# Kernel optimization log

Measured on AMD Instinct MI355X. Metric: run time of the kernel, lower is better.

## Reference

```python
import jax, jax.numpy as jnp
import numpy as np

LN2 = jnp.log(jnp.float32(2.0))
ALPHA = 0.5          # alpha_pool = [0.5]
A_BITS = 8           # activation bit width (BIT_TYPE_A)
W_BITS = 8           # weight bit width (BIT_TYPE_W)
EPS = 1e-8


def round_ln(x):
    # 'round' branch: floor(log2(x)) then pick nearer power of two
    y = jnp.floor(jnp.log(x) / LN2)
    up = (x - 2.0 ** y) > (2.0 ** (y + 1.0) - x)
    return y + up.astype(x.dtype)


def fq_act_asym(x, bits=A_BITS):
    # per-tensor asymmetric uniform fake-quant (QAct min-max observer)
    qmax = 2 ** bits - 1
    xmin = jnp.minimum(x.min(), 0.0)
    xmax = jnp.maximum(x.max(), 0.0)
    scale = jnp.maximum((xmax - xmin) / qmax, EPS)
    zp = jnp.round(-xmin / scale)
    q = jnp.clip(jnp.round(x / scale) + zp, 0, qmax)
    return (q - zp) * scale


def fq_act_sym(x, bits=A_BITS):
    # per-tensor symmetric fake-quant (qact1 with asymmetric=False)
    qmax = 2 ** (bits - 1) - 1
    scale = jnp.maximum(jnp.abs(x).max() / qmax, EPS)
    q = jnp.clip(jnp.round(x / scale), -qmax - 1, qmax)
    return q * scale


def fq_weight(w, bits=W_BITS):
    # per-output-channel symmetric weight fake-quant (QLinear)
    qmax = 2 ** (bits - 1) - 1
    scale = jnp.maximum(jnp.abs(w).max(axis=1, keepdims=True) / qmax, EPS)
    q = jnp.clip(jnp.round(w / scale), -qmax - 1, qmax)
    return q * scale


def setup_inputs() -> dict:
    key = jax.random.key(0)
    ks = jax.random.split(key, 5)
    B, N, C, H = 64, 197, 768, 3072
    x = jax.random.normal(ks[0], (B, N, C), dtype=jnp.float32)
    w1 = jax.random.normal(ks[1], (H, C), dtype=jnp.float32) * 0.02
    b1 = jax.random.normal(ks[2], (H,), dtype=jnp.float32) * 0.02
    w2 = jax.random.normal(ks[3], (C, H), dtype=jnp.float32) * 0.02
    b2 = jax.random.normal(ks[4], (C,), dtype=jnp.float32) * 0.02
    return {"x": x, "w1": w1, "b1": b1, "w2": w2, "b2": b2}


def reference(x, w1, b1, w2, b2):
    # ---- smoothquant power-of-two channel scale (fc1 input channels) ----
    global_max_x = jnp.abs(x).max(axis=(0, 1))      # [C]
    max_weight = jnp.abs(w1).max(axis=0)            # [C]
    cs = global_max_x ** ALPHA / max_weight ** (1.0 - ALPHA)
    cs = 2.0 ** round_ln(cs)                        # snap to power of two
    x_smoothed = x / cs[None, None, :]
    w1_smoothed = w1 * cs[None, :]
    # ---- qact0 -> fc1 (8-bit fake-quant GEMM) ----
    xq = fq_act_asym(x_smoothed)
    h = jnp.einsum('bnc,hc->bnh', xq, fq_weight(w1_smoothed)) + b1
    # ---- act (exact GELU, nn.GELU default) -> qact1 (symmetric) ----
    h = jax.nn.gelu(h, approximate=False)
    hq = fq_act_sym(h)
    # ---- fc2 -> qact2 ----
    out = jnp.einsum('bnh,ch->bnc', hq, fq_weight(w2)) + b2
    out = fq_act_asym(out)
    return out
```

## Files before the change

kernel.cpp:

```cpp
#include <hip/hip_runtime.h>
#include <cstdint>
#include <cstddef>

typedef int v4i __attribute__((ext_vector_type(4)));

#define DI static __device__ __forceinline__

DI unsigned fmap(float f){ unsigned b=__float_as_uint(f); return (b&0x80000000u)? ~b : (b|0x80000000u); }
DI float funmap(unsigned u){ return (u&0x80000000u)? __uint_as_float(u&0x7fffffffu) : __uint_as_float(~u); }
DI float gelu_f(float x){ return 0.5f*x*(1.0f+erff(x*0.70710678118654752440f)); }

constexpr int Mtok = 12608;
constexpr int Cdim = 768;
constexpr int Hdim = 3072;
constexpr int MP   = 12672;

__global__ void k_init(unsigned* scal, unsigned* xminU, unsigned* xmaxU, unsigned* wmaxU){
    int t = blockIdx.x*256 + threadIdx.x;
    if (t < Cdim){
        xminU[t] = fmap(__builtin_inff());
        xmaxU[t] = fmap(-__builtin_inff());
        wmaxU[t] = fmap(0.0f);
    }
    if (t == 0){
        scal[0] = fmap(0.0f);
        scal[1] = fmap(__builtin_inff());
        scal[2] = fmap(-__builtin_inff());
    }
}

__global__ void k_colstats_x(const float* __restrict__ x, unsigned* xminU, unsigned* xmaxU){
    int t = threadIdx.x;
    float mn0= __builtin_inff(), mn1= __builtin_inff(), mn2= __builtin_inff();
    float mx0=-__builtin_inff(), mx1=-__builtin_inff(), mx2=-__builtin_inff();
    for (int r = blockIdx.x; r < Mtok; r += gridDim.x){
        const float* row = x + (size_t)r*Cdim;
        float v0=row[t], v1=row[t+256], v2=row[t+512];
        mn0=fminf(mn0,v0); mx0=fmaxf(mx0,v0);
        mn1=fminf(mn1,v1); mx1=fmaxf(mx1,v1);
        mn2=fminf(mn2,v2); mx2=fmaxf(mx2,v2);
    }
    atomicMin(&xminU[t      ], fmap(mn0)); atomicMax(&xmaxU[t      ], fmap(mx0));
    atomicMin(&xminU[t+256  ], fmap(mn1)); atomicMax(&xmaxU[t+256  ], fmap(mx1));
    atomicMin(&xminU[t+512  ], fmap(mn2)); atomicMax(&xmaxU[t+512  ], fmap(mx2));
}

__global__ void k_colmax_w1(const float* __restrict__ w1, unsigned* wmaxU){
    int t = threadIdx.x;
    float m0=0.f, m1=0.f, m2=0.f;
    for (int r = blockIdx.x; r < Hdim; r += gridDim.x){
        const float* row = w1 + (size_t)r*Cdim;
        m0=fmaxf(m0,fabsf(row[t]));
        m1=fmaxf(m1,fabsf(row[t+256]));
        m2=fmaxf(m2,fabsf(row[t+512]));
    }
    atomicMax(&wmaxU[t      ], fmap(m0));
    atomicMax(&wmaxU[t+256  ], fmap(m1));
    atomicMax(&wmaxU[t+512  ], fmap(m2));
}

__global__ void k_scale0(const unsigned* xminU, const unsigned* xmaxU, const unsigned* wmaxU,
                         float* cs, unsigned* scal){
    __shared__ float smn[256], smx[256];
    int t = threadIdx.x;
    float lmn =  __builtin_inff(), lmx = -__builtin_inff();
    #pragma unroll
    for (int j = 0; j < 3; ++j){
        int c = t + j*256;
        float xn = funmap(xminU[c]), xm = funmap(xmaxU[c]), wm = funmap(wmaxU[c]);
        float g  = fmaxf(fabsf(xn), fabsf(xm));
        float csr = powf(g, 0.5f) / powf(wm, 0.5f);
        float y = floorf(logf(csr) / 0.6931471805599453f);
        float p = exp2f(y);
        float c2 = exp2f(y + (((csr - p) > (2.0f*p - csr)) ? 1.0f : 0.0f));
        cs[c] = c2;
        lmn = fminf(lmn, xn / c2);
        lmx = fmaxf(lmx, xm / c2);
    }
    smn[t]=lmn; smx[t]=lmx; __syncthreads();
    for (int s=128; s; s>>=1){
        if (t < s){ smn[t]=fminf(smn[t],smn[t+s]); smx[t]=fmaxf(smx[t],smx[t+s]); }
        __syncthreads();
    }
    if (t == 0){
        float xmin_t = fminf(smn[0], 0.0f);
        float xmax_t = fmaxf(smx[0], 0.0f);
        float sc = fmaxf((xmax_t - xmin_t)/255.0f, 1e-8f);
        float zp = rintf(-xmin_t/sc);
        float* fs = (float*)scal;
        fs[8] = sc; fs[9] = zp;
    }
}

__global__ void k_quant_w1(const float* __restrict__ w1, const float* __restrict__ cs,
                           const unsigned* scal, int8_t* __restrict__ qw1,
                           float* sa1, int* icorr1){
    __shared__ float sm[256];
    __shared__ int   si[256];
    int h = blockIdx.x, t = threadIdx.x;
    const float* wr = w1 + (size_t)h*Cdim;
    float v0 = wr[t]*cs[t], v1 = wr[t+256]*cs[t+256], v2 = wr[t+512]*cs[t+512];
    float am = fmaxf(fabsf(v0), fmaxf(fabsf(v1), fabsf(v2)));
    sm[t]=am; __syncthreads();
    for (int s=128; s; s>>=1){ if (t<s) sm[t]=fmaxf(sm[t],sm[t+s]); __syncthreads(); }
    float scale = fmaxf(sm[0]/127.0f, 1e-8f);
    float q0 = fminf(fmaxf(rintf(v0/scale), -128.0f), 127.0f);
    float q1 = fminf(fmaxf(rintf(v1/scale), -128.0f), 127.0f);
    float q2 = fminf(fmaxf(rintf(v2/scale), -128.0f), 127.0f);
    qw1[(size_t)h*Cdim + t      ] = (int8_t)q0;
    qw1[(size_t)h*Cdim + t + 256] = (int8_t)q1;
    qw1[(size_t)h*Cdim + t + 512] = (int8_t)q2;
    si[t] = (int)q0 + (int)q1 + (int)q2; __syncthreads();
    for (int s=128; s; s>>=1){ if (t<s) si[t]+=si[t+s]; __syncthreads(); }
    if (t == 0){
        const float* fs = (const float*)scal;
        sa1[h]    = fs[8]*scale;
        icorr1[h] = (128 - (int)fs[9]) * si[0];
    }
}

__global__ void k_quant_w2(const float* __restrict__ w2, int8_t* __restrict__ qw2, float* sa2){
    __shared__ float sm[256];
    int c = blockIdx.x, t = threadIdx.x;
    const float* wr = w2 + (size_t)c*Hdim;
    float v[12]; float am = 0.f;
    #pragma unroll
    for (int j=0;j<12;++j){ v[j]=wr[t + j*256]; am=fmaxf(am,fabsf(v[j])); }
    sm[t]=am; __syncthreads();
    for (int s=128; s; s>>=1){ if (t<s) sm[t]=fmaxf(sm[t],sm[t+s]); __syncthreads(); }
    float scale = fmaxf(sm[0]/127.0f, 1e-8f);
    #pragma unroll
    for (int j=0;j<12;++j){
        float q = fminf(fmaxf(rintf(v[j]/scale), -128.0f), 127.0f);
        qw2[(size_t)c*Hdim + t + j*256] = (int8_t)q;
    }
    if (t == 0) sa2[c] = scale;
}

__global__ void k_quant_x(const float* __restrict__ x, const float* __restrict__ cs,
                          const unsigned* scal, int8_t* __restrict__ qxs){
    int idx = blockIdx.x*256 + threadIdx.x;
    const int total = Mtok*(Cdim/4);
    if (idx >= total) return;
    const float* fs = (const float*)scal;
    float sc = fs[8], zp = fs[9];
    float4 v = ((const float4*)x)[idx];
    int cb = (idx % (Cdim/4))*4;
    float q0 = fminf(fmaxf(rintf((v.x/cs[cb+0])/sc)+zp, 0.f), 255.f);
    float q1 = fminf(fmaxf(rintf((v.y/cs[cb+1])/sc)+zp, 0.f), 255.f);
    float q2 = fminf(fmaxf(rintf((v.z/cs[cb+2])/sc)+zp, 0.f), 255.f);
    float q3 = fminf(fmaxf(rintf((v.w/cs[cb+3])/sc)+zp, 0.f), 255.f);
    uint32_t pack =  (uint32_t)(uint8_t)((int)q0-128)
                  | ((uint32_t)(uint8_t)((int)q1-128) << 8)
                  | ((uint32_t)(uint8_t)((int)q2-128) << 16)
                  | ((uint32_t)(uint8_t)((int)q3-128) << 24);
    ((uint32_t*)qxs)[idx] = pack;
}

#define GLL(src,dst) __builtin_amdgcn_global_load_lds( \
    (const __attribute__((address_space(1))) unsigned*)(src), \
    (__attribute__((address_space(3))) unsigned*)(dst), 16, 0, 0)

template<int KSTEPS, int MODE, int NY>
__global__ __launch_bounds__(256)
void k_gemm(const int8_t* __restrict__ A, const int8_t* __restrict__ Bw, int N,
            const float* __restrict__ sa, const int* __restrict__ icorr,
            const float* __restrict__ bias, const unsigned* __restrict__ scal,
            int8_t* __restrict__ qout, float* __restrict__ fout, _Float16* __restrict__ hout,
            unsigned* __restrict__ r0, unsigned* __restrict__ r1)
{
    constexpr int K = KSTEPS*64;
    __shared__ __align__(16) int8_t LDSB[24576];
    __shared__ float sred[8];
    int t = threadIdx.x, lane = t & 63, wid = t >> 6;
    int wr = wid >> 1, wc = wid & 1;

    int nwg = gridDim.x;
    int q8 = nwg >> 3, r8 = nwg & 7;
    int xcd = blockIdx.x & 7, li = blockIdx.x >> 3;
    int swz = (xcd < r8 ? xcd*(q8+1) : r8*(q8+1) + (xcd - r8)*q8) + li;
    int bx = swz / NY, by = swz % NY;
    size_t brow = (size_t)bx * 128;
    int bcol = by * 128;

    int srow = t >> 2;
    int schunk = (t & 3) ^ ((srow >> 1) & 3);
    const int8_t* ga0 = A  + (brow + srow)*(size_t)K + schunk*16;

    const int8_t* gB = Bw + (size_t)(bcol + wc*64 + (lane & 15))*K + ((lane >> 4) << 4);

    int rsw  = ((lane >> 4) ^ ((lane >> 1) & 3)) << 4;
    int aoff = ((wr*64 + (lane & 15)) << 6) + rsw;

    float sav[4], bbv[4]; int icv[4]; float sh = 0.f;
    #pragma unroll
    for (int n=0;n<4;++n){
        int col = bcol + wc*64 + n*16 + (lane & 15);
        sav[n] = sa[col];
        bbv[n] = bias[col];
        icv[n] = (MODE == 2) ? 0 : icorr[col];
    }
    if (MODE == 1 || MODE == 2) sh = fmaxf(funmap(*scal)/127.0f, 1e-8f);
    asm volatile("" ::: "memory");

#define STAGE(sb, ks) do{ \
    const int8_t* pa_ = ga0 + (ks)*64; \
    int8_t* ld_ = LDSB + (sb)*8192 + t*16; \
    GLL(pa_,                ld_); \
    GLL(pa_ + (size_t)64*K, ld_ + 4096); \
}while(0)

    v4i acc[4][4] = {};
    v4i bcur[4];

    STAGE(0,0);
    __builtin_amdgcn_sched_barrier(0);
    #pragma unroll
    for (int n=0;n<4;++n) bcur[n] = *(const v4i*)(gB + (size_t)n*(16*K));
    __builtin_amdgcn_sched_barrier(0);
    STAGE(1,1);

#define ITER(cur, ks, WAITN, HASB, HASSTAGE) do{ \
    asm volatile("s_waitcnt vmcnt(" #WAITN ")" ::: "memory"); \
    __builtin_amdgcn_s_barrier(); \
    v4i bn_[4]; \
    if (HASB){ \
        _Pragma("unroll") \
        for (int n_=0;n_<4;++n_) bn_[n_] = *(const v4i*)(gB + (size_t)n_*(16*K) + ((ks)+1)*64); \
    } \
    __builtin_amdgcn_sched_barrier(0); \
    if (HASSTAGE) STAGE(((cur)+2)%3, (ks)+2); \
    const int8_t* bp_ = LDSB + (cur)*8192; \
    v4i a_[4]; \
    _Pragma("unroll") \
    for (int m_=0;m_<4;++m_) a_[m_] = *(const v4i*)(bp_ + aoff + (m_<<10)); \
    asm volatile("s_waitcnt lgkmcnt(0)" ::: "memory"); \
    __builtin_amdgcn_sched_barrier(0); \
    __builtin_amdgcn_s_setprio(1); \
    _Pragma("unroll") \
    for (int m_=0;m_<4;++m_) \
        _Pragma("unroll") \
        for (int n_=0;n_<4;++n_) \
            acc[m_][n_] = __builtin_amdgcn_mfma_i32_16x16x64_i8(a_[m_], bcur[n_], acc[m_][n_], 0, 0, 0); \
    __builtin_amdgcn_s_setprio(0); \
    if (HASB){ \
        _Pragma("unroll") \
        for (int n_=0;n_<4;++n_) bcur[n_] = bn_[n_]; \
    } \
}while(0)

    constexpr int MAING = KSTEPS/3 - 1;
    for (int kg = 0; kg < MAING; ++kg){
        int ks = kg*3;
        ITER(0, ks,   2, true, true);
        ITER(1, ks+1, 2, true, true);
        ITER(2, ks+2, 2, true, true);
    }
    ITER(0, KSTEPS-3, 2, true,  true);
    ITER(1, KSTEPS-2, 2, true,  false);
    ITER(2, KSTEPS-1, 0, false, false);
#undef ITER
#undef STAGE

    int rl = (lane >> 4) * 4;
    if (MODE == 0){
        float amax = 0.f;
        #pragma unroll
        for (int n=0;n<4;++n){
            #pragma unroll
            for (int m=0;m<4;++m){
                size_t row = brow + wr*64 + m*16 + rl;
                #pragma unroll
                for (int r=0;r<4;++r){
                    if (row + r < (size_t)Mtok){
                        float g = gelu_f(sav[n]*(float)(acc[m][n][r] + icv[n]) + bbv[n]);
                        amax = fmaxf(amax, fabsf(g));
                    }
                }
            }
        }
        #pragma unroll
        for (int off=32; off; off>>=1) amax = fmaxf(amax, __shfl_down(amax, off));
        if (lane == 0) sred[wid] = amax;
        __syncthreads();
        if (t == 0) atomicMax(r0, fmap(fmaxf(fmaxf(sred[0],sred[1]), fmaxf(sred[2],sred[3]))));
    } else if (MODE == 1){
        #pragma unroll
        for (int n=0;n<4;++n){
            int col = bcol + wc*64 + n*16 + (lane & 15);
            #pragma unroll
            for (int m=0;m<4;++m){
                size_t row = brow + wr*64 + m*16 + rl;
                #pragma unroll
                for (int r=0;r<4;++r){
                    if (row + r < (size_t)Mtok){
                        float g = gelu_f(sav[n]*(float)(acc[m][n][r] + icv[n]) + bbv[n]);
                        float qv = fminf(fmaxf(rintf(g/sh), -128.0f), 127.0f);
                        qout[(row + r)*(size_t)N + col] = (int8_t)qv;
                    }
                }
            }
        }
    } else if (MODE == 3){
        float amax = 0.f;
        _Float16* hb = hout + ((size_t)(bx*NY + by))*16384 + wid*4096 + lane*4;
        #pragma unroll
        for (int n=0;n<4;++n){
            #pragma unroll
            for (int m=0;m<4;++m){
                size_t row = brow + wr*64 + m*16 + rl;
                union { _Float16 h4[4]; uint2 u2; } pk;
                #pragma unroll
                for (int r=0;r<4;++r){
                    float g = gelu_f(sav[n]*(float)(acc[m][n][r] + icv[n]) + bbv[n]);
                    if (row + r < (size_t)Mtok) amax = fmaxf(amax, fabsf(g));
                    pk.h4[r] = (_Float16)g;
                }
                *(uint2*)(hb + (n*4+m)*256) = pk.u2;
            }
        }
        #pragma unroll
        for (int off=32; off; off>>=1) amax = fmaxf(amax, __shfl_down(amax, off));
        if (lane == 0) sred[wid] = amax;
        __syncthreads();
        if (t == 0) atomicMax(r0, fmap(fmaxf(fmaxf(sred[0],sred[1]), fmaxf(sred[2],sred[3]))));
    } else {
        float lmin =  __builtin_inff(), lmax = -__builtin_inff();
        float* ob = fout + ((size_t)(bx*NY + by))*16384 + wid*4096 + lane*4;
        #pragma unroll
        for (int n=0;n<4;++n){
            float s = sh * sav[n];
            #pragma unroll
            for (int m=0;m<4;++m){
                size_t row = brow + wr*64 + m*16 + rl;
                float4 o4;
                #pragma unroll
                for (int r=0;r<4;++r){
                    float o = s*(float)acc[m][n][r] + bbv[n];
                    if (row + r < (size_t)Mtok){ lmin = fminf(lmin, o); lmax = fmaxf(lmax, o); }
                    ((float*)&o4)[r] = o;
                }
                *(float4*)(ob + (n*4+m)*256) = o4;
            }
        }
        #pragma unroll
        for (int off=32; off; off>>=1){
            lmin = fminf(lmin, __shfl_down(lmin, off));
            lmax = fmaxf(lmax, __shfl_down(lmax, off));
        }
        if (lane == 0){ sred[wid] = lmin; sred[4+wid] = lmax; }
        __syncthreads();
        if (t == 0){
            atomicMin(r0, fmap(fminf(fminf(sred[0],sred[1]), fminf(sred[2],sred[3]))));
            atomicMax(r1, fmap(fmaxf(fmaxf(sred[4],sred[5]), fmaxf(sred[6],sred[7]))));
        }
    }
}

__global__ void k_requant(const _Float16* __restrict__ h, const unsigned* __restrict__ scal,
                          int8_t* __restrict__ qh){
    int idx = blockIdx.x*256 + threadIdx.x;
    const int total = Mtok*(Hdim/8);
    if (idx >= total) return;
    float sh = fmaxf(funmap(scal[0])/127.0f, 1e-8f);
    int R  = idx / 384;
    int cb = (idx - R*384) * 8;
    int bx = R >> 7, r0 = R & 127;
    int by = cb >> 7, c0 = cb & 127;
    int wid2 = (r0 >> 6)*2 + (c0 >> 6);
    int m = (r0 >> 4) & 3, n = (c0 >> 4) & 3;
    int lane2 = ((r0 >> 2) & 3)*16 + (c0 & 15);
    int r = r0 & 3;
    const _Float16* p = h + ((size_t)(bx*24 + by))*16384 + wid2*4096 + (n*4+m)*256 + lane2*4 + r;
    uint32_t lo = 0, hi = 0;
    #pragma unroll
    for (int j=0;j<4;++j){
        float q = fminf(fmaxf(rintf((float)p[4*j]/sh), -128.0f), 127.0f);
        lo |= ((uint32_t)(uint8_t)(int)q) << (8*j);
    }
    #pragma unroll
    for (int j=0;j<4;++j){
        float q = fminf(fmaxf(rintf((float)p[4*(4+j)]/sh), -128.0f), 127.0f);
        hi |= ((uint32_t)(uint8_t)(int)q) << (8*j);
    }
    uint2 pk; pk.x = lo; pk.y = hi;
    ((uint2*)qh)[idx] = pk;
}

__global__ void k_final(const float* __restrict__ outpre, const unsigned* __restrict__ scal,
                        float* __restrict__ out){
    int idx = blockIdx.x*256 + threadIdx.x;
    const int total = Mtok*(Cdim/4);
    if (idx >= total) return;
    float omin = fminf(funmap(scal[1]), 0.0f);
    float omax = fmaxf(funmap(scal[2]), 0.0f);
    float sc = fmaxf((omax - omin)/255.0f, 1e-8f);
    float zp = rintf(-omin/sc);
    int R  = idx / 192;
    int cb = (idx - R*192) * 4;
    int bx = R >> 7, r0 = R & 127;
    int by = cb >> 7, c0 = cb & 127;
    int wid2 = (r0 >> 6)*2 + (c0 >> 6);
    int m = (r0 >> 4) & 3, n = (c0 >> 4) & 3;
    int lane2 = ((r0 >> 2) & 3)*16 + (c0 & 15);
    int r = r0 & 3;
    const float* p = outpre + ((size_t)(bx*6 + by))*16384 + wid2*4096 + (n*4+m)*256 + lane2*4 + r;
    float4 v;
    v.x = p[0]; v.y = p[4]; v.z = p[8]; v.w = p[12];
    v.x = (fminf(fmaxf(rintf(v.x/sc)+zp, 0.f), 255.f) - zp)*sc;
    v.y = (fminf(fmaxf(rintf(v.y/sc)+zp, 0.f), 255.f) - zp)*sc;
    v.z = (fminf(fmaxf(rintf(v.z/sc)+zp, 0.f), 255.f) - zp)*sc;
    v.w = (fminf(fmaxf(rintf(v.w/sc)+zp, 0.f), 255.f) - zp)*sc;
    ((float4*)out)[idx] = v;
}

extern "C" void kernel_launch(void* const* d_in, const int* in_sizes, int n_in,
                              void* d_out, int out_size, void* d_ws, size_t ws_size,
                              hipStream_t stream)
{
    if (n_in < 5) return;
    const float* x  = (const float*)d_in[0];
    const float* w1 = (const float*)d_in[1];
    const float* b1 = (const float*)d_in[2];
    const float* w2 = (const float*)d_in[3];
    const float* b2 = (const float*)d_in[4];
    float* out = (float*)d_out;

    uint8_t* w = (uint8_t*)d_ws;
    size_t off = 0;
    unsigned* scal  = (unsigned*)(w + off); off += 256;
    unsigned* xminU = (unsigned*)(w + off); off += 3072;
    unsigned* xmaxU = (unsigned*)(w + off); off += 3072;
    unsigned* wmaxU = (unsigned*)(w + off); off += 3072;
    float*    cs    = (float*)   (w + off); off += 3072;
    float*    sa1   = (float*)   (w + off); off += 12288;
    int*      icorr1= (int*)     (w + off); off += 12288;
    float*    sa2   = (float*)   (w + off); off += 3072;
    off = (off + 255) & ~(size_t)255;
    int8_t*   qw1   = (int8_t*)  (w + off); off += (size_t)Hdim*Cdim;
    int8_t*   qw2   = (int8_t*)  (w + off); off += (size_t)Cdim*Hdim;
    int8_t*   qxs   = (int8_t*)  (w + off); off += (size_t)MP*Cdim;
    int8_t*   qh    = (int8_t*)  (w + off); off += (size_t)MP*Hdim;
    size_t off_big = off;
    float*    outpre= (float*)   (w + off_big);
    _Float16* hbuf  = (_Float16*)(w + off_big);
    size_t need_3g  = off_big + (size_t)99*6*16384*4;
    size_t need_h16 = off_big + (size_t)99*24*16384*2;
    if (ws_size < need_3g) return;
    bool use_h16 = (ws_size >= need_h16);

    k_init<<<3, 256, 0, stream>>>(scal, xminU, xmaxU, wmaxU);
    k_colstats_x<<<512, 256, 0, stream>>>(x, xminU, xmaxU);
    k_colmax_w1<<<512, 256, 0, stream>>>(w1, wmaxU);
    k_scale0<<<1, 256, 0, stream>>>(xminU, xmaxU, wmaxU, cs, scal);
    k_quant_w1<<<Hdim, 256, 0, stream>>>(w1, cs, scal, qw1, sa1, icorr1);
    k_quant_w2<<<Cdim, 256, 0, stream>>>(w2, qw2, sa2);
    k_quant_x<<<(Mtok*(Cdim/4) + 255)/256, 256, 0, stream>>>(x, cs, scal, qxs);

    if (use_h16){
        k_gemm<12,3,24><<<2376, 256, 0, stream>>>(qxs, qw1, Hdim, sa1, icorr1, b1, scal,
                                                  nullptr, nullptr, hbuf, &scal[0], nullptr);
        k_requant<<<(Mtok*(Hdim/8) + 255)/256, 256, 0, stream>>>(hbuf, scal, qh);
    } else {
        k_gemm<12,0,24><<<2376, 256, 0, stream>>>(qxs, qw1, Hdim, sa1, icorr1, b1, scal,
                                                  nullptr, nullptr, nullptr, &scal[0], nullptr);
        k_gemm<12,1,24><<<2376, 256, 0, stream>>>(qxs, qw1, Hdim, sa1, icorr1, b1, scal,
                                                  qh, nullptr, nullptr, nullptr, nullptr);
    }
    k_gemm<48,2,6><<<594, 256, 0, stream>>>(qh, qw2, Cdim, sa2, nullptr, b2, scal,
                                            nullptr, outpre, nullptr, &scal[1], &scal[2]);

    k_final<<<(Mtok*(Cdim/4) + 255)/256, 256, 0, stream>>>(outpre, scal, out);
}
```

Measured before the change: 442.5 us.

## Replace triple-buffered GEMM pipeline with double-buffered 128-K stages and fast erf

Replaces the hand-scheduled three-stage LDS pipeline (64-wide K steps, explicit vmcnt waits, register-prefetched B) with a simpler double-buffered loop over 128-wide K stages, using an XOR swizzle across 8 chunks and __syncthreads between stages. It also adds a launch-bounds occupancy hint of 3 blocks per CU and swaps erff for an Abramowitz-Stegun polynomial erf in GELU. The aim is fewer barriers per K and cheaper epilogue math. The cost is less fine-grained overlap, with B loads no longer prefetched a step ahead, and an erf approximation with about 1e-7 error that could flip rounding on a few quantized values.

```diff
diff --git a/kernel.cpp b/kernel.cpp
--- a/kernel.cpp
+++ b/kernel.cpp
@@ -8,7 +8,15 @@
 
 DI unsigned fmap(float f){ unsigned b=__float_as_uint(f); return (b&0x80000000u)? ~b : (b|0x80000000u); }
 DI float funmap(unsigned u){ return (u&0x80000000u)? __uint_as_float(u&0x7fffffffu) : __uint_as_float(~u); }
-DI float gelu_f(float x){ return 0.5f*x*(1.0f+erff(x*0.70710678118654752440f)); }
+
+DI float erf_fast(float x){
+    float ax = fabsf(x);
+    float t  = __builtin_amdgcn_rcpf(1.0f + 0.3275911f*ax);
+    float p  = t*(0.254829592f + t*(-0.284496736f + t*(1.421413741f + t*(-1.453152027f + t*1.061405429f))));
+    float r  = 1.0f - p*__expf(-ax*ax);
+    return copysignf(r, x);
+}
+DI float gelu_f(float x){ return 0.5f*x*(1.0f + erf_fast(x*0.70710678118654752440f)); }
 
 constexpr int Mtok = 12608;
 constexpr int Cdim = 768;
@@ -161,19 +169,20 @@
     (const __attribute__((address_space(1))) unsigned*)(src), \
     (__attribute__((address_space(3))) unsigned*)(dst), 16, 0, 0)
 
-template<int KSTEPS, int MODE, int NY>
-__global__ __launch_bounds__(256)
+template<int KDIM, int MODE, int NY>
+__global__ __launch_bounds__(256, 3)
 void k_gemm(const int8_t* __restrict__ A, const int8_t* __restrict__ Bw, int N,
             const float* __restrict__ sa, const int* __restrict__ icorr,
             const float* __restrict__ bias, const unsigned* __restrict__ scal,
             int8_t* __restrict__ qout, float* __restrict__ fout, _Float16* __restrict__ hout,
             unsigned* __restrict__ r0, unsigned* __restrict__ r1)
 {
-    constexpr int K = KSTEPS*64;
-    __shared__ __align__(16) int8_t LDSB[24576];
+    constexpr int NST = KDIM/128;
+    __shared__ __align__(16) int8_t LDSB[2][16384];
     __shared__ float sred[8];
     int t = threadIdx.x, lane = t & 63, wid = t >> 6;
     int wr = wid >> 1, wc = wid & 1;
+    int l15 = lane & 15, lhi = lane >> 4, l7 = lane & 7;
 
     int nwg = gridDim.x;
     int q8 = nwg >> 3, r8 = nwg & 7;
@@ -183,86 +192,66 @@
     size_t brow = (size_t)bx * 128;
     int bcol = by * 128;
 
-    int srow = t >> 2;
-    int schunk = (t & 3) ^ ((srow >> 1) & 3);
-    const int8_t* ga0 = A  + (brow + srow)*(size_t)K + schunk*16;
-
-    const int8_t* gB = Bw + (size_t)(bcol + wc*64 + (lane & 15))*K + ((lane >> 4) << 4);
-
-    int rsw  = ((lane >> 4) ^ ((lane >> 1) & 3)) << 4;
-    int aoff = ((wr*64 + (lane & 15)) << 6) + rsw;
+    int srow   = t >> 3;
+    int schunk = (t & 7) ^ (srow & 7);
+    const int8_t* ga0 = A + (size_t)(brow + srow)*KDIM + schunk*16;
+
+    const int8_t* gB = Bw + (size_t)(bcol + wc*64 + l15)*KDIM + (lhi << 4);
+
+    int arow = (wr*64 + l15) * 128;
 
     float sav[4], bbv[4]; int icv[4]; float sh = 0.f;
     #pragma unroll
     for (int n=0;n<4;++n){
-        int col = bcol + wc*64 + n*16 + (lane & 15);
+        int col = bcol + wc*64 + n*16 + l15;
         sav[n] = sa[col];
         bbv[n] = bias[col];
         icv[n] = (MODE == 2) ? 0 : icorr[col];
     }
     if (MODE == 1 || MODE == 2) sh = fmaxf(funmap(*scal)/127.0f, 1e-8f);
-    asm volatile("" ::: "memory");
-
-#define STAGE(sb, ks) do{ \
-    const int8_t* pa_ = ga0 + (ks)*64; \
-    int8_t* ld_ = LDSB + (sb)*8192 + t*16; \
-    GLL(pa_,                ld_); \
-    GLL(pa_ + (size_t)64*K, ld_ + 4096); \
+
+#define STAGE(buf, s) do{ \
+    const int8_t* p_ = ga0 + (size_t)(s)*128; \
+    int8_t* l_ = LDSB[buf] + t*16; \
+    GLL(p_,                   l_); \
+    GLL(p_ + (size_t)32*KDIM, l_ + 4096); \
+    GLL(p_ + (size_t)64*KDIM, l_ + 8192); \
+    GLL(p_ + (size_t)96*KDIM, l_ + 12288); \
 }while(0)
 
     v4i acc[4][4] = {};
-    v4i bcur[4];
-
-    STAGE(0,0);
-    __builtin_amdgcn_sched_barrier(0);
-    #pragma unroll
-    for (int n=0;n<4;++n) bcur[n] = *(const v4i*)(gB + (size_t)n*(16*K));
-    __builtin_amdgcn_sched_barrier(0);
-    STAGE(1,1);
-
-#define ITER(cur, ks, WAITN, HASB, HASSTAGE) do{ \
-    asm volatile("s_waitcnt vmcnt(" #WAITN ")" ::: "memory"); \
-    __builtin_amdgcn_s_barrier(); \
-    v4i bn_[4]; \
-    if (HASB){ \
-        _Pragma("unroll") \
-        for (int n_=0;n_<4;++n_) bn_[n_] = *(const v4i*)(gB + (size_t)n_*(16*K) + ((ks)+1)*64); \
-    } \
-    __builtin_amdgcn_sched_barrier(0); \
-    if (HASSTAGE) STAGE(((cur)+2)%3, (ks)+2); \
-    const int8_t* bp_ = LDSB + (cur)*8192; \
-    v4i a_[4]; \
-    _Pragma("unroll") \
-    for (int m_=0;m_<4;++m_) a_[m_] = *(const v4i*)(bp_ + aoff + (m_<<10)); \
-    asm volatile("s_waitcnt lgkmcnt(0)" ::: "memory"); \
-    __builtin_amdgcn_sched_barrier(0); \
-    __builtin_amdgcn_s_setprio(1); \
-    _Pragma("unroll") \
-    for (int m_=0;m_<4;++m_) \
-        _Pragma("unroll") \
-        for (int n_=0;n_<4;++n_) \
-            acc[m_][n_] = __builtin_amdgcn_mfma_i32_16x16x64_i8(a_[m_], bcur[n_], acc[m_][n_], 0, 0, 0); \
-    __builtin_amdgcn_s_setprio(0); \
-    if (HASB){ \
-        _Pragma("unroll") \
-        for (int n_=0;n_<4;++n_) bcur[n_] = bn_[n_]; \
-    } \
-}while(0)
-
-    constexpr int MAING = KSTEPS/3 - 1;
-    for (int kg = 0; kg < MAING; ++kg){
-        int ks = kg*3;
-        ITER(0, ks,   2, true, true);
-        ITER(1, ks+1, 2, true, true);
-        ITER(2, ks+2, 2, true, true);
-    }
-    ITER(0, KSTEPS-3, 2, true,  true);
-    ITER(1, KSTEPS-2, 2, true,  false);
-    ITER(2, KSTEPS-1, 0, false, false);
-#undef ITER
+    STAGE(0, 0);
+    __syncthreads();
+
+    for (int s = 0; s < NST; ++s){
+        int cur = s & 1;
+        v4i bb[4][2];
+        #pragma unroll
+        for (int n=0;n<4;++n)
+            #pragma unroll
+            for (int kc=0;kc<2;++kc)
+                bb[n][kc] = *(const v4i*)(gB + (size_t)n*(16*KDIM) + s*128 + kc*64);
+        if (s + 1 < NST) STAGE(cur^1, s+1);
+        v4i aa[4][2];
+        #pragma unroll
+        for (int m=0;m<4;++m)
+            #pragma unroll
+            for (int kc=0;kc<2;++kc)
+                aa[m][kc] = *(const v4i*)(LDSB[cur] + arow + (m<<11) + (((kc*4 + lhi) ^ l7) << 4));
+        __builtin_amdgcn_s_setprio(1);
+        #pragma unroll
+        for (int kc=0;kc<2;++kc)
+            #pragma unroll
+            for (int m=0;m<4;++m)
+                #pragma unroll
+                for (int n=0;n<4;++n)
+                    acc[m][n] = __builtin_amdgcn_mfma_i32_16x16x64_i8(aa[m][kc], bb[n][kc], acc[m][n], 0, 0, 0);
+        __builtin_amdgcn_s_setprio(0);
+        __syncthreads();
+    }
 #undef STAGE
 
-    int rl = (lane >> 4) * 4;
+    int rl = lhi * 4;
     if (MODE == 0){
         float amax = 0.f;
         #pragma unroll
@@ -287,7 +276,7 @@
     } else if (MODE == 1){
         #pragma unroll
         for (int n=0;n<4;++n){
-            int col = bcol + wc*64 + n*16 + (lane & 15);
+            int col = bcol + wc*64 + n*16 + l15;
             #pragma unroll
             for (int m=0;m<4;++m){
                 size_t row = brow + wr*64 + m*16 + rl;
@@ -458,17 +447,17 @@
     k_quant_x<<<(Mtok*(Cdim/4) + 255)/256, 256, 0, stream>>>(x, cs, scal, qxs);
 
     if (use_h16){
-        k_gemm<12,3,24><<<2376, 256, 0, stream>>>(qxs, qw1, Hdim, sa1, icorr1, b1, scal,
-                                                  nullptr, nullptr, hbuf, &scal[0], nullptr);
+        k_gemm<768,3,24><<<2376, 256, 0, stream>>>(qxs, qw1, Hdim, sa1, icorr1, b1, scal,
+                                                   nullptr, nullptr, hbuf, &scal[0], nullptr);
         k_requant<<<(Mtok*(Hdim/8) + 255)/256, 256, 0, stream>>>(hbuf, scal, qh);
     } else {
-        k_gemm<12,0,24><<<2376, 256, 0, stream>>>(qxs, qw1, Hdim, sa1, icorr1, b1, scal,
-                                                  nullptr, nullptr, nullptr, &scal[0], nullptr);
-        k_gemm<12,1,24><<<2376, 256, 0, stream>>>(qxs, qw1, Hdim, sa1, icorr1, b1, scal,
-                                                  qh, nullptr, nullptr, nullptr, nullptr);
-    }
-    k_gemm<48,2,6><<<594, 256, 0, stream>>>(qh, qw2, Cdim, sa2, nullptr, b2, scal,
-                                            nullptr, outpre, nullptr, &scal[1], &scal[2]);
+        k_gemm<768,0,24><<<2376, 256, 0, stream>>>(qxs, qw1, Hdim, sa1, icorr1, b1, scal,
+                                                   nullptr, nullptr, nullptr, &scal[0], nullptr);
+        k_gemm<768,1,24><<<2376, 256, 0, stream>>>(qxs, qw1, Hdim, sa1, icorr1, b1, scal,
+                                                   qh, nullptr, nullptr, nullptr, nullptr);
+    }
+    k_gemm<3072,2,6><<<594, 256, 0, stream>>>(qh, qw2, Cdim, sa2, nullptr, b2, scal,
+                                              nullptr, outpre, nullptr, &scal[1], &scal[2]);
 
     k_final<<<(Mtok*(Cdim/4) + 255)/256, 256, 0, stream>>>(outpre, scal, out);
 }
```

Result: faster. 408.0 us (-7.8%).
